# Performance work log

Hardware: AMD Instinct MI355X
Metric: run time of the kernel (lower is better)

The kernel has to match this reference:

```python
import jax, jax.numpy as jnp
import numpy as np

# Four fixed 3x3 Sobel-like kernels (same as the torch source), applied depthwise per channel.
_K = np.stack([
    np.array([[-1, 0, 1], [-2, 0, 2], [-1, 0, 1]], dtype=np.float32),
    np.array([[1, 2, 1], [0, 0, 0], [-1, -2, -1]], dtype=np.float32),
    np.array([[2, 1, 0], [1, 0, -1], [0, -1, -2]], dtype=np.float32),
    np.array([[0, -1, -2], [1, 0, -1], [2, 1, 0]], dtype=np.float32),
])  # (4,3,3)
SOBEL_KERNELS = jnp.asarray(_K)[:, None, :, :]  # (4,1,3,3) OIHW


def setup_inputs() -> dict:
    key = jax.random.key(0)
    x = jax.random.normal(key, (32, 3, 512, 512), dtype=jnp.float32)
    return {"x": x}


def reference(x) -> jnp.ndarray:
    B, C, H, W = x.shape
    # Apply each of the 4 kernels to every channel independently (depthwise):
    # fold channels into batch, conv with 4 output filters, abs, sum over the 4.
    xf = x.reshape(B * C, 1, H, W)
    edges = jax.lax.conv_general_dilated(
        xf, SOBEL_KERNELS,
        window_strides=(1, 1), padding="SAME",
        dimension_numbers=("NCHW", "OIHW", "NCHW"),
    )  # (B*C, 4, H, W)
    sobel_out = jnp.sum(jnp.abs(edges), axis=1).reshape(B, C, H, W)
    s = jax.nn.sigmoid(sobel_out)
    # hard threshold: <= 0.5 -> 0, > 0.5 -> 1
    return jnp.where(s > 0.5, jnp.float32(1.0), jnp.float32(0.0))
```

## Files before the change

kernel.cpp:

```cpp
#include <hip/hip_runtime.h>


#define IMG_H 512
#define IMG_W 512

typedef float f32x4 __attribute__((ext_vector_type(4)));

__global__ __launch_bounds__(256) void sobel_thresh_kernel(
    const float* __restrict__ x, float* __restrict__ out) {
    int t    = blockIdx.x * blockDim.x + threadIdx.x;
    int lane = t & 63;
    int wid  = t >> 6;
    int hg   = wid & 127;
    int img  = wid >> 7;
    int h0   = hg << 2;
    int wA   = lane << 2;
    int wB   = 256 + (lane << 2);

    const float* base = x + (size_t)img * (IMG_H * IMG_W);

    float A[6][6], B[6][6];
#pragma unroll
    for (int r = 0; r < 6; ++r) {
        int h = h0 - 1 + r;
        if (h >= 0 && h < IMG_H) {
            const float* rp = base + h * IMG_W;
            f32x4 a = *reinterpret_cast<const f32x4*>(rp + wA);
            f32x4 b = *reinterpret_cast<const f32x4*>(rp + wB);
            A[r][1] = a.x; A[r][2] = a.y; A[r][3] = a.z; A[r][4] = a.w;
            B[r][1] = b.x; B[r][2] = b.y; B[r][3] = b.z; B[r][4] = b.w;
            float a_l = __shfl_up(a.w, 1);
            float a_r = __shfl_down(a.x, 1);
            float b_l = __shfl_up(b.w, 1);
            float b_r = __shfl_down(b.x, 1);
            float seam_r = __shfl(b.x, 0);
            float seam_l = __shfl(a.w, 63);
            A[r][0] = (lane == 0)  ? 0.0f   : a_l;
            A[r][5] = (lane == 63) ? seam_r : a_r;
            B[r][0] = (lane == 0)  ? seam_l : b_l;
            B[r][5] = (lane == 63) ? 0.0f   : b_r;
        } else {
#pragma unroll
            for (int i = 0; i < 6; ++i) { A[r][i] = 0.0f; B[r][i] = 0.0f; }
        }
    }

    float* obase = out + (size_t)img * (IMG_H * IMG_W) + (size_t)h0 * IMG_W;
#pragma unroll
    for (int i = 0; i < 4; ++i) {
        f32x4 oA, oB;
#pragma unroll
        for (int half = 0; half < 2; ++half) {
            const float (*ra)[6] = half ? B : A;
            f32x4* o = half ? &oB : &oA;
#pragma unroll
            for (int j = 0; j < 4; ++j) {
                float t0 = ra[i][j],     t1 = ra[i][j + 1],     t2 = ra[i][j + 2];
                float m0 = ra[i + 1][j],                        m2 = ra[i + 1][j + 2];
                float b0 = ra[i + 2][j], b1 = ra[i + 2][j + 1], b2 = ra[i + 2][j + 2];
                float e0 = (t2 - t0) + 2.0f * (m2 - m0) + (b2 - b0);
                float e1 = (t0 + 2.0f * t1 + t2) - (b0 + 2.0f * b1 + b2);
                float e2 = 2.0f * t0 + t1 + m0 - m2 - b1 - 2.0f * b2;
                float e3 = -t1 - 2.0f * t2 + m0 - m2 + 2.0f * b0 + b1;
                float s = fabsf(e0) + fabsf(e1) + fabsf(e2) + fabsf(e3);
                (*o)[j] = (s > 0.0f) ? 1.0f : 0.0f;
            }
        }
        float* op = obase + i * IMG_W;
        __builtin_nontemporal_store(oA, reinterpret_cast<f32x4*>(op + wA));
        __builtin_nontemporal_store(oB, reinterpret_cast<f32x4*>(op + wB));
    }
}

extern "C" void kernel_launch(void* const* d_in, const int* in_sizes, int n_in,
                              void* d_out, int out_size, void* d_ws, size_t ws_size,
                              hipStream_t stream) {
    const float* x = (const float*)d_in[0];
    float* out = (float*)d_out;
    int total = 96 * 128 * 64;
    int block = 256;
    int grid = total / block;
    sobel_thresh_kernel<<<grid, block, 0, stream>>>(x, out);
}
```

Measured before the change: 37.75 us.

## Process 8 rows per wave with rolling row window and swizzled block order

Each wave now produces 8 output rows instead of 4, keeping a 3-row rolling register window, so the halo re-read overhead drops from 6/4 to 10/8 rows loaded per output row. Block indices are remapped so consecutive blocks land on different XCDs in an interleaved pattern, and the e2/e3 diagonal responses are derived algebraically from e0/e1 to cut arithmetic. The grid halves to 1536 blocks, which reduces parallelism and per-wave latency hiding with fewer waves in flight.

```diff
diff --git a/kernel.cpp b/kernel.cpp
--- a/kernel.cpp
+++ b/kernel.cpp
@@ -6,66 +6,73 @@
 
 typedef float f32x4 __attribute__((ext_vector_type(4)));
 
+__device__ __forceinline__ void load_row(const float* __restrict__ base, int h,
+                                         int wA, int wB, int lane,
+                                         float (&A)[6], float (&B)[6]) {
+    if (h >= 0 && h < IMG_H) {
+        const float* rp = base + h * IMG_W;
+        f32x4 a = *reinterpret_cast<const f32x4*>(rp + wA);
+        f32x4 b = *reinterpret_cast<const f32x4*>(rp + wB);
+        A[1] = a.x; A[2] = a.y; A[3] = a.z; A[4] = a.w;
+        B[1] = b.x; B[2] = b.y; B[3] = b.z; B[4] = b.w;
+        float a_l = __shfl_up(a.w, 1);
+        float a_r = __shfl_down(a.x, 1);
+        float b_l = __shfl_up(b.w, 1);
+        float b_r = __shfl_down(b.x, 1);
+        float seam_r = __shfl(b.x, 0);
+        float seam_l = __shfl(a.w, 63);
+        A[0] = (lane == 0)  ? 0.0f   : a_l;
+        A[5] = (lane == 63) ? seam_r : a_r;
+        B[0] = (lane == 0)  ? seam_l : b_l;
+        B[5] = (lane == 63) ? 0.0f   : b_r;
+    } else {
+#pragma unroll
+        for (int i = 0; i < 6; ++i) { A[i] = 0.0f; B[i] = 0.0f; }
+    }
+}
+
+__device__ __forceinline__ void sobel4(const float (&T)[6], const float (&M)[6],
+                                       const float (&Bt)[6], f32x4& o) {
+#pragma unroll
+    for (int j = 0; j < 4; ++j) {
+        float t0 = T[j], t1 = T[j + 1], t2 = T[j + 2];
+        float m0 = M[j],                m2 = M[j + 2];
+        float b0 = Bt[j], b1 = Bt[j + 1], b2 = Bt[j + 2];
+        float e0 = (t2 - t0) + 2.0f * (m2 - m0) + (b2 - b0);
+        float e1 = (t0 + 2.0f * t1 + t2) - (b0 + 2.0f * b1 + b2);
+        float e2 = 0.5f * (e1 - e0) + (t0 - b2);
+        float e3 = -0.5f * (e0 + e1) + (b0 - t2);
+        float s = fabsf(e0) + fabsf(e1) + fabsf(e2) + fabsf(e3);
+        o[j] = (s > 0.0f) ? 1.0f : 0.0f;
+    }
+}
+
 __global__ __launch_bounds__(256) void sobel_thresh_kernel(
     const float* __restrict__ x, float* __restrict__ out) {
-    int t    = blockIdx.x * blockDim.x + threadIdx.x;
+    int bid  = blockIdx.x;
+    int sbid = (bid & 7) * 192 + (bid >> 3);
+    int t    = sbid * 256 + (int)threadIdx.x;
     int lane = t & 63;
     int wid  = t >> 6;
-    int hg   = wid & 127;
-    int img  = wid >> 7;
-    int h0   = hg << 2;
+    int hg   = wid & 63;
+    int img  = wid >> 6;
+    int h0   = hg << 3;
     int wA   = lane << 2;
     int wB   = 256 + (lane << 2);
 
     const float* base = x + (size_t)img * (IMG_H * IMG_W);
+    float* obase = out + (size_t)img * (IMG_H * IMG_W) + (size_t)h0 * IMG_W;
 
-    float A[6][6], B[6][6];
+    float WA[3][6], WB[3][6];
+    load_row(base, h0 - 1, wA, wB, lane, WA[0], WB[0]);
+    load_row(base, h0,     wA, wB, lane, WA[1], WB[1]);
+
 #pragma unroll
-    for (int r = 0; r < 6; ++r) {
-        int h = h0 - 1 + r;
-        if (h >= 0 && h < IMG_H) {
-            const float* rp = base + h * IMG_W;
-            f32x4 a = *reinterpret_cast<const f32x4*>(rp + wA);
-            f32x4 b = *reinterpret_cast<const f32x4*>(rp + wB);
-            A[r][1] = a.x; A[r][2] = a.y; A[r][3] = a.z; A[r][4] = a.w;
-            B[r][1] = b.x; B[r][2] = b.y; B[r][3] = b.z; B[r][4] = b.w;
-            float a_l = __shfl_up(a.w, 1);
-            float a_r = __shfl_down(a.x, 1);
-            float b_l = __shfl_up(b.w, 1);
-            float b_r = __shfl_down(b.x, 1);
-            float seam_r = __shfl(b.x, 0);
-            float seam_l = __shfl(a.w, 63);
-            A[r][0] = (lane == 0)  ? 0.0f   : a_l;
-            A[r][5] = (lane == 63) ? seam_r : a_r;
-            B[r][0] = (lane == 0)  ? seam_l : b_l;
-            B[r][5] = (lane == 63) ? 0.0f   : b_r;
-        } else {
-#pragma unroll
-            for (int i = 0; i < 6; ++i) { A[r][i] = 0.0f; B[r][i] = 0.0f; }
-        }
-    }
-
-    float* obase = out + (size_t)img * (IMG_H * IMG_W) + (size_t)h0 * IMG_W;
-#pragma unroll
-    for (int i = 0; i < 4; ++i) {
+    for (int i = 0; i < 8; ++i) {
+        load_row(base, h0 + 1 + i, wA, wB, lane, WA[(i + 2) % 3], WB[(i + 2) % 3]);
         f32x4 oA, oB;
-#pragma unroll
-        for (int half = 0; half < 2; ++half) {
-            const float (*ra)[6] = half ? B : A;
-            f32x4* o = half ? &oB : &oA;
-#pragma unroll
-            for (int j = 0; j < 4; ++j) {
-                float t0 = ra[i][j],     t1 = ra[i][j + 1],     t2 = ra[i][j + 2];
-                float m0 = ra[i + 1][j],                        m2 = ra[i + 1][j + 2];
-                float b0 = ra[i + 2][j], b1 = ra[i + 2][j + 1], b2 = ra[i + 2][j + 2];
-                float e0 = (t2 - t0) + 2.0f * (m2 - m0) + (b2 - b0);
-                float e1 = (t0 + 2.0f * t1 + t2) - (b0 + 2.0f * b1 + b2);
-                float e2 = 2.0f * t0 + t1 + m0 - m2 - b1 - 2.0f * b2;
-                float e3 = -t1 - 2.0f * t2 + m0 - m2 + 2.0f * b0 + b1;
-                float s = fabsf(e0) + fabsf(e1) + fabsf(e2) + fabsf(e3);
-                (*o)[j] = (s > 0.0f) ? 1.0f : 0.0f;
-            }
-        }
+        sobel4(WA[i % 3], WA[(i + 1) % 3], WA[(i + 2) % 3], oA);
+        sobel4(WB[i % 3], WB[(i + 1) % 3], WB[(i + 2) % 3], oB);
         float* op = obase + i * IMG_W;
         __builtin_nontemporal_store(oA, reinterpret_cast<f32x4*>(op + wA));
         __builtin_nontemporal_store(oB, reinterpret_cast<f32x4*>(op + wB));
@@ -77,8 +84,7 @@
                               hipStream_t stream) {
     const float* x = (const float*)d_in[0];
     float* out = (float*)d_out;
-    int total = 96 * 128 * 64;
+    int grid = 1536;
     int block = 256;
-    int grid = total / block;
     sobel_thresh_kernel<<<grid, block, 0, stream>>>(x, out);
 }
```

Measured after the change: 38.70 us. 2.5% more time.
